# Optimization experiments

Measured on AMD Instinct MI355X. Metric: run time of the kernel, lower is better.

The kernel has to match this reference:

```python
import jax, jax.numpy as jnp
import numpy as np

D_MODEL = 1024
H = 16
D_K = D_MODEL // H


def setup_inputs() -> dict:
    key = jax.random.key(0)
    ks = jax.random.split(key, 9)
    s = 0.02
    x = jax.random.normal(ks[0], (2, 2048, D_MODEL), dtype=jnp.float32)
    Wq = jax.random.normal(ks[1], (D_MODEL, D_MODEL), dtype=jnp.float32) * s
    bq = jax.random.normal(ks[2], (D_MODEL,), dtype=jnp.float32) * s
    Wk = jax.random.normal(ks[3], (D_MODEL, D_MODEL), dtype=jnp.float32) * s
    bk = jax.random.normal(ks[4], (D_MODEL,), dtype=jnp.float32) * s
    Wv = jax.random.normal(ks[5], (D_MODEL, D_MODEL), dtype=jnp.float32) * s
    bv = jax.random.normal(ks[6], (D_MODEL,), dtype=jnp.float32) * s
    Wo = jax.random.normal(ks[7], (D_MODEL, D_MODEL), dtype=jnp.float32) * s
    bo = jax.random.normal(ks[8], (D_MODEL,), dtype=jnp.float32) * s
    return {"x": x, "Wq": Wq, "bq": bq, "Wk": Wk, "bk": bk,
            "Wv": Wv, "bv": bv, "Wo": Wo, "bo": bo}


def reference(x, Wq, bq, Wk, bk, Wv, bv, Wo, bo):
    b, s, _ = x.shape
    scale = 1.0 / jnp.sqrt(jnp.float32(D_K))
    # projections; [b, s, d] -> [b, h, s, d_k]
    def split_heads(t):
        return t.reshape(b, s, H, D_K).transpose(0, 2, 1, 3)
    q = split_heads(x @ Wq + bq)
    k = split_heads(x @ Wk + bk)
    v = split_heads(x @ Wv + bv)
    scores = jnp.einsum('bhqd,bhkd->bhqk', q, k) * scale  # [b,h,s,s]
    attn = jax.nn.softmax(scores, axis=-1)
    ctx = jnp.einsum('bhqk,bhkd->bhqd', attn, v)
    ctx = ctx.transpose(0, 2, 1, 3).reshape(b, s, D_MODEL)
    return ctx @ Wo + bo + x
```

## Files before the change

### kernel.cpp

```cpp
#include <hip/hip_runtime.h>
#include <hip/hip_bf16.h>
#include <stdint.h>

#define D_MODEL 1024
#define NH 16
#define DK 64
#define S_LEN 2048

typedef __attribute__((ext_vector_type(8))) __bf16 bf16x8;
typedef __attribute__((ext_vector_type(4))) float f32x4;

#define GLOBAL_AS __attribute__((address_space(1)))
#define LDS_AS    __attribute__((address_space(3)))

__device__ __forceinline__ void async16(const ushort* g, ushort* l) {
    __builtin_amdgcn_global_load_lds(
        (const GLOBAL_AS uint32_t*)(uintptr_t)(const void*)g,
        (LDS_AS uint32_t*)(uint32_t)(uintptr_t)(void*)l,
        16, 0, 0);
}

__device__ __forceinline__ ushort f2bf(float f) {
    union { float f; uint32_t u; } v; v.f = f;
    uint32_t lsb = (v.u >> 16) & 1u;
    return (ushort)((v.u + 0x7fffu + lsb) >> 16);
}

__device__ __forceinline__ uint32_t packbf(float a, float b) {
    union { float f; uint32_t u; } x, y; x.f = a; y.f = b;
    return ((x.u + 0x8000u) >> 16) | ((y.u + 0x8000u) & 0xffff0000u);
}

__device__ __forceinline__ bf16x8 ldfrag(const ushort* p) {
    union { uint4 u; bf16x8 b; } cv;
    cv.u = *(const uint4*)p;
    return cv.b;
}


__global__ void cvt_x_kernel(const float* __restrict__ x, ushort* __restrict__ xb) {
    int i = blockIdx.x * 256 + threadIdx.x;
    float4 v = ((const float4*)x)[i];
    ushort4 o;
    o.x = f2bf(v.x); o.y = f2bf(v.y); o.z = f2bf(v.z); o.w = f2bf(v.w);
    ((ushort4*)xb)[i] = o;
}

__global__ void transpose_cvt4_kernel(
    const float* __restrict__ W0, const float* __restrict__ W1,
    const float* __restrict__ W2, const float* __restrict__ W3,
    ushort* __restrict__ D0, ushort* __restrict__ D1,
    ushort* __restrict__ D2, ushort* __restrict__ D3) {
    const float* W; ushort* D;
    switch (blockIdx.z) {
        case 0: W = W0; D = D0; break;
        case 1: W = W1; D = D1; break;
        case 2: W = W2; D = D2; break;
        default: W = W3; D = D3; break;
    }
    __shared__ float tile[32][33];
    int bx = blockIdx.x * 32, by = blockIdx.y * 32;
    int tx = threadIdx.x, ty = threadIdx.y;
#pragma unroll
    for (int j = 0; j < 32; j += 8)
        tile[ty + j][tx] = W[(size_t)(by + ty + j) * D_MODEL + bx + tx];
    __syncthreads();
#pragma unroll
    for (int j = 0; j < 32; j += 8)
        D[(size_t)(bx + ty + j) * D_MODEL + by + tx] = f2bf(tile[tx][ty + j]);
}

__global__ void cvt_bias_kernel(const float* __restrict__ bq, const float* __restrict__ bk,
                                const float* __restrict__ bv, float* __restrict__ out) {
    int i = blockIdx.x * 256 + threadIdx.x;
    float v = (i < 1024) ? bq[i] : (i < 2048 ? bk[i - 1024] : bv[i - 2048]);
    out[i] = v;
}

template <int MODE>
__global__ __launch_bounds__(256) void gemm_kernel(
    const ushort* __restrict__ A, const ushort* __restrict__ Bt,
    const float* __restrict__ bias,
    ushort* __restrict__ outQ, ushort* __restrict__ outK, ushort* __restrict__ outVt,
    const float* __restrict__ xres, float* __restrict__ outF) {
    constexpr int BN = (MODE == 0) ? 128 : 64;
    constexpr int NI = (MODE == 0) ? 4 : 2;
    __shared__ __align__(16) ushort sA[2][128 * 32];
    __shared__ __align__(16) ushort sB[2][BN * 32];
    const int tid = threadIdx.x;
    const int wave = tid >> 6, lane = tid & 63;
    const int lr = lane & 15, lq = lane >> 4;
    const int srow = lane >> 2;
    const int sc = (lane & 3) ^ ((lane >> 4) & 3);

    const int bid = blockIdx.x;
    const int xcd = bid & 7, lb = bid >> 3;
    int bx, by;
    if (MODE == 0) { bx = xcd * 3 + (lb % 3); by = lb / 3; }
    else           { bx = xcd * 2 + (lb & 1); by = lb >> 1; }
    const int blockM = by * 128;
    const int blockN = bx * BN;
    const int waveM = (wave >> 1) * 64;
    const int waveN = (MODE == 0) ? (wave & 1) * 64 : (wave & 1) * 32;

    auto stage = [&](int k0, int b) {
#pragma unroll
        for (int t = 0; t < 2; t++) {
            int row = wave * 32 + t * 16 + srow;
            async16(&A[(size_t)(blockM + row) * D_MODEL + k0 + sc * 8],
                    &sA[b][(wave * 32 + t * 16) * 32]);
        }
        if (MODE == 0) {
#pragma unroll
            for (int t = 0; t < 2; t++) {
                int row = wave * 32 + t * 16 + srow;
                async16(&Bt[(size_t)(blockN + row) * D_MODEL + k0 + sc * 8],
                        &sB[b][(wave * 32 + t * 16) * 32]);
            }
        } else {
            int row = wave * 16 + srow;
            async16(&Bt[(size_t)(blockN + row) * D_MODEL + k0 + sc * 8],
                    &sB[b][wave * 16 * 32]);
        }
    };

    f32x4 acc[4][NI] = {};
    const int swz = (lq ^ ((lr >> 2) & 3)) * 8;

    stage(0, 0);
    __syncthreads();
#pragma unroll 2
    for (int k = 0; k < 32; k++) {
        const int cur = k & 1;
        if (k < 31) stage((k + 1) * 32, cur ^ 1);
        bf16x8 af[4], bfr[NI];
#pragma unroll
        for (int mi = 0; mi < 4; mi++)
            af[mi] = ldfrag(&sA[cur][(waveM + mi * 16 + lr) * 32 + swz]);
#pragma unroll
        for (int ni = 0; ni < NI; ni++)
            bfr[ni] = ldfrag(&sB[cur][(waveN + ni * 16 + lr) * 32 + swz]);
#pragma unroll
        for (int mi = 0; mi < 4; mi++)
#pragma unroll
            for (int ni = 0; ni < NI; ni++)
                acc[mi][ni] = __builtin_amdgcn_mfma_f32_16x16x32_bf16(
                    af[mi], bfr[ni], acc[mi][ni], 0, 0, 0);
        __syncthreads();
    }

#pragma unroll
    for (int mi = 0; mi < 4; mi++) {
#pragma unroll
        for (int ni = 0; ni < NI; ni++) {
#pragma unroll
            for (int r = 0; r < 4; r++) {
                int m = blockM + waveM + mi * 16 + lq * 4 + r;
                int n = blockN + waveN + ni * 16 + lr;
                float v = acc[mi][ni][r] + bias[n];
                if (MODE == 0) {
                    int which = n >> 10, c = n & 1023;
                    int h = c >> 6, d = c & 63;
                    int b = m >> 11, s = m & 2047;
                    size_t bh = (size_t)(b * NH + h);
                    if (which == 0)
                        outQ[(bh * S_LEN + s) * DK + d] = f2bf(v * 0.125f);
                    else if (which == 1)
                        outK[(bh * S_LEN + s) * DK + d] = f2bf(v);
                    else
                        outVt[(bh * DK + d) * S_LEN + s] = f2bf(v);
                } else {
                    size_t idx = (size_t)m * D_MODEL + n;
                    outF[idx] = v + xres[idx];
                }
            }
        }
    }
}

__global__ __launch_bounds__(256, 3) void attn_kernel(
    const ushort* __restrict__ Q, const ushort* __restrict__ Km,
    const ushort* __restrict__ Vt, ushort* __restrict__ ctx) {
    const int bid = blockIdx.x;
    const int xcd = bid & 7, lb = bid >> 3;
    const int bh = xcd * 4 + (lb & 3);
    const int qt = lb >> 2;
    const int q0 = qt * 128;
    __shared__ __align__(16) ushort sQ[128 * 64];
    __shared__ __align__(16) ushort sK[64 * 64];
    __shared__ __align__(16) ushort sV[64 * 64];
    __shared__ __align__(16) ushort sP[4 * 32 * 72];
    const int tid = threadIdx.x;
    const int wave = tid >> 6, lane = tid & 63;
    const int lr = lane & 15, lq = lane >> 4;
    const int srow = lane >> 3, sp = lane & 7;
    const ushort* Qh = Q + (size_t)bh * S_LEN * DK;
    const ushort* Kh = Km + (size_t)bh * S_LEN * DK;
    const ushort* Vh = Vt + (size_t)bh * DK * S_LEN;
    ushort* sPw = &sP[wave * 32 * 72];

#pragma unroll
    for (int t = 0; t < 4; t++) {
        int row = wave * 32 + t * 8 + srow;
        int c = sp ^ (row & 7);
        async16(&Qh[(size_t)(q0 + row) * DK + c * 8], &sQ[(wave * 32 + t * 8) * 64]);
    }
    __syncthreads();

    bf16x8 qf[2][2];
#pragma unroll
    for (int mi = 0; mi < 2; mi++)
#pragma unroll
        for (int kk = 0; kk < 2; kk++)
            qf[mi][kk] = ldfrag(&sQ[(wave * 32 + mi * 16 + lr) * 64 +
                                    (((kk * 4 + lq) ^ (lr & 7)) * 8)]);

    f32x4 cacc[2][4] = {};
    float lsum[2] = {0.f, 0.f};

    for (int k0 = 0; k0 < S_LEN; k0 += 64) {
        __syncthreads();
#pragma unroll
        for (int t = 0; t < 2; t++) {
            int row = wave * 16 + t * 8 + srow;
            int c = sp ^ (row & 7);
            async16(&Kh[(size_t)(k0 + row) * DK + c * 8], &sK[(wave * 16 + t * 8) * 64]);
            async16(&Vh[(size_t)row * S_LEN + k0 + c * 8], &sV[(wave * 16 + t * 8) * 64]);
        }
        __syncthreads();

        f32x4 sacc[2][4] = {};
#pragma unroll
        for (int kk = 0; kk < 2; kk++) {
            bf16x8 kf[4];
            int swz = ((kk * 4 + lq) ^ (lr & 7)) * 8;
#pragma unroll
            for (int nj = 0; nj < 4; nj++)
                kf[nj] = ldfrag(&sK[(nj * 16 + lr) * 64 + swz]);
#pragma unroll
            for (int mi = 0; mi < 2; mi++)
#pragma unroll
                for (int nj = 0; nj < 4; nj++)
                    sacc[mi][nj] = __builtin_amdgcn_mfma_f32_16x16x32_bf16(
                        kf[nj], qf[mi][kk], sacc[mi][nj], 0, 0, 0);
        }

#pragma unroll
        for (int mi = 0; mi < 2; mi++) {
#pragma unroll
            for (int nj = 0; nj < 4; nj++) {
                float p0 = __expf(sacc[mi][nj][0]);
                float p1 = __expf(sacc[mi][nj][1]);
                float p2 = __expf(sacc[mi][nj][2]);
                float p3 = __expf(sacc[mi][nj][3]);
                lsum[mi] += (p0 + p1) + (p2 + p3);
                uint2 w;
                w.x = packbf(p0, p1);
                w.y = packbf(p2, p3);
                *(uint2*)&sPw[(mi * 16 + lr) * 72 + nj * 16 + lq * 4] = w;
            }
        }

#pragma unroll
        for (int ks = 0; ks < 2; ks++) {
            bf16x8 pf[2], vf[4];
#pragma unroll
            for (int mi = 0; mi < 2; mi++)
                pf[mi] = ldfrag(&sPw[(mi * 16 + lr) * 72 + ks * 32 + lq * 8]);
            int swz = ((ks * 4 + lq) ^ (lr & 7)) * 8;
#pragma unroll
            for (int nd = 0; nd < 4; nd++)
                vf[nd] = ldfrag(&sV[(nd * 16 + lr) * 64 + swz]);
#pragma unroll
            for (int mi = 0; mi < 2; mi++)
#pragma unroll
                for (int nd = 0; nd < 4; nd++)
                    cacc[mi][nd] = __builtin_amdgcn_mfma_f32_16x16x32_bf16(
                        pf[mi], vf[nd], cacc[mi][nd], 0, 0, 0);
        }
    }

    float inv[2];
#pragma unroll
    for (int mi = 0; mi < 2; mi++) {
        float l = lsum[mi];
        l += __shfl_xor(l, 16);
        l += __shfl_xor(l, 32);
        inv[mi] = 1.f / l;
    }
    float invr[2][4];
#pragma unroll
    for (int mi = 0; mi < 2; mi++)
#pragma unroll
        for (int r = 0; r < 4; r++)
            invr[mi][r] = __shfl(inv[mi], lq * 4 + r);

    const int b = bh >> 4, h = bh & 15;
#pragma unroll
    for (int mi = 0; mi < 2; mi++)
#pragma unroll
        for (int nd = 0; nd < 4; nd++)
#pragma unroll
            for (int r = 0; r < 4; r++) {
                int qrow = q0 + wave * 32 + mi * 16 + lq * 4 + r;
                int d = nd * 16 + lr;
                float v = cacc[mi][nd][r] * invr[mi][r];
                ctx[(size_t)(b * S_LEN + qrow) * D_MODEL + h * DK + d] = f2bf(v);
            }
}


extern "C" void kernel_launch(void* const* d_in, const int* in_sizes, int n_in,
                              void* d_out, int out_size, void* d_ws, size_t ws_size,
                              hipStream_t stream) {
    const float* x  = (const float*)d_in[0];
    const float* Wq = (const float*)d_in[1];
    const float* bq = (const float*)d_in[2];
    const float* Wk = (const float*)d_in[3];
    const float* bk = (const float*)d_in[4];
    const float* Wv = (const float*)d_in[5];
    const float* bv = (const float*)d_in[6];
    const float* Wo = (const float*)d_in[7];
    const float* bo = (const float*)d_in[8];

    char* ws = (char*)d_ws;
    ushort* xb    = (ushort*)(ws);
    ushort* wqkv  = (ushort*)(ws + (8ull  << 20));
    ushort* wo_t  = (ushort*)(ws + (14ull << 20));
    ushort* qbuf  = (ushort*)(ws + (16ull << 20));
    ushort* kbuf  = (ushort*)(ws + (24ull << 20));
    ushort* vtb   = (ushort*)(ws + (32ull << 20));
    ushort* ctx   = (ushort*)(ws + (40ull << 20));
    float*  biasq = (float*)(ws + (48ull << 20));

    cvt_x_kernel<<<4096, 256, 0, stream>>>(x, xb);
    transpose_cvt4_kernel<<<dim3(32, 32, 4), dim3(32, 8), 0, stream>>>(
        Wq, Wk, Wv, Wo, wqkv, wqkv + 1024 * 1024, wqkv + 2 * 1024 * 1024, wo_t);
    cvt_bias_kernel<<<12, 256, 0, stream>>>(bq, bk, bv, biasq);

    gemm_kernel<0><<<768, 256, 0, stream>>>(
        xb, wqkv, biasq, qbuf, kbuf, vtb, nullptr, nullptr);
    attn_kernel<<<512, 256, 0, stream>>>(qbuf, kbuf, vtb, ctx);
    gemm_kernel<1><<<512, 256, 0, stream>>>(
        ctx, wo_t, bo, nullptr, nullptr, nullptr, x, (float*)d_out);
}
```

Measured before the change: 216.5 us.

## Triple-buffer GEMMs, halve attention q-tile, use exp2 and MFMA row sums

The GEMM kernel moves from two to three LDS stages. It prefetches two k-steps ahead and replaces __syncthreads with a vmcnt-bounded barrier, and the output-projection block mapping is remapped across XCDs. The attention kernel shrinks the query tile to 64 rows with 16 per wave and reuses the Q LDS slot for P. It folds log2(e) into the Q scale so it can use a raw v_exp_f32, and computes softmax row sums with an extra MFMA against a ones vector in place of scalar adds and shuffles. The aims are more overlap of loads with MFMA, more blocks for occupancy, and less VALU work. In exchange K/V traffic per query doubles, and the vmcnt counts must match the number of loads issued.

```diff
diff --git a/kernel.cpp b/kernel.cpp
--- a/kernel.cpp
+++ b/kernel.cpp
@@ -18,6 +18,17 @@
         (const GLOBAL_AS uint32_t*)(uintptr_t)(const void*)g,
         (LDS_AS uint32_t*)(uint32_t)(uintptr_t)(void*)l,
         16, 0, 0);
+}
+
+template <int N>
+__device__ __forceinline__ void pipe_barrier() {
+    asm volatile("s_waitcnt vmcnt(%0)\n\ts_barrier" :: "n"(N) : "memory");
+}
+
+__device__ __forceinline__ float fast_exp2(float x) {
+    float r;
+    asm("v_exp_f32 %0, %1" : "=v"(r) : "v"(x));
+    return r;
 }
 
 __device__ __forceinline__ ushort f2bf(float f) {
@@ -85,8 +96,9 @@
     const float* __restrict__ xres, float* __restrict__ outF) {
     constexpr int BN = (MODE == 0) ? 128 : 64;
     constexpr int NI = (MODE == 0) ? 4 : 2;
-    __shared__ __align__(16) ushort sA[2][128 * 32];
-    __shared__ __align__(16) ushort sB[2][BN * 32];
+    constexpr int NS = (MODE == 0) ? 4 : 3;
+    __shared__ __align__(16) ushort sA[3][128 * 32];
+    __shared__ __align__(16) ushort sB[3][BN * 32];
     const int tid = threadIdx.x;
     const int wave = tid >> 6, lane = tid & 63;
     const int lr = lane & 15, lq = lane >> 4;
@@ -97,56 +109,63 @@
     const int xcd = bid & 7, lb = bid >> 3;
     int bx, by;
     if (MODE == 0) { bx = xcd * 3 + (lb % 3); by = lb / 3; }
-    else           { bx = xcd * 2 + (lb & 1); by = lb >> 1; }
+    else           { by = xcd * 4 + (lb & 3); bx = lb >> 2; }
     const int blockM = by * 128;
     const int blockN = bx * BN;
     const int waveM = (wave >> 1) * 64;
     const int waveN = (MODE == 0) ? (wave & 1) * 64 : (wave & 1) * 32;
 
-    auto stage = [&](int k0, int b) {
+    auto stage = [&](int k0, ushort* a, ushort* b) {
 #pragma unroll
         for (int t = 0; t < 2; t++) {
             int row = wave * 32 + t * 16 + srow;
             async16(&A[(size_t)(blockM + row) * D_MODEL + k0 + sc * 8],
-                    &sA[b][(wave * 32 + t * 16) * 32]);
+                    &a[(wave * 32 + t * 16) * 32]);
         }
         if (MODE == 0) {
 #pragma unroll
             for (int t = 0; t < 2; t++) {
                 int row = wave * 32 + t * 16 + srow;
                 async16(&Bt[(size_t)(blockN + row) * D_MODEL + k0 + sc * 8],
-                        &sB[b][(wave * 32 + t * 16) * 32]);
+                        &b[(wave * 32 + t * 16) * 32]);
             }
         } else {
             int row = wave * 16 + srow;
             async16(&Bt[(size_t)(blockN + row) * D_MODEL + k0 + sc * 8],
-                    &sB[b][wave * 16 * 32]);
+                    &b[wave * 16 * 32]);
         }
     };
 
     f32x4 acc[4][NI] = {};
     const int swz = (lq ^ ((lr >> 2) & 3)) * 8;
 
-    stage(0, 0);
+    stage(0, sA[0], sB[0]);
+    stage(32, sA[1], sB[1]);
     __syncthreads();
-#pragma unroll 2
+
+    int cur = 0;
+#pragma unroll 4
     for (int k = 0; k < 32; k++) {
-        const int cur = k & 1;
-        if (k < 31) stage((k + 1) * 32, cur ^ 1);
+        int nx = cur + 2; if (nx >= 3) nx -= 3;
+        if (k + 2 < 32) stage((k + 2) * 32, sA[nx], sB[nx]);
+        const ushort* a = sA[cur];
+        const ushort* b = sB[cur];
         bf16x8 af[4], bfr[NI];
 #pragma unroll
         for (int mi = 0; mi < 4; mi++)
-            af[mi] = ldfrag(&sA[cur][(waveM + mi * 16 + lr) * 32 + swz]);
+            af[mi] = ldfrag(&a[(waveM + mi * 16 + lr) * 32 + swz]);
 #pragma unroll
         for (int ni = 0; ni < NI; ni++)
-            bfr[ni] = ldfrag(&sB[cur][(waveN + ni * 16 + lr) * 32 + swz]);
+            bfr[ni] = ldfrag(&b[(waveN + ni * 16 + lr) * 32 + swz]);
 #pragma unroll
         for (int mi = 0; mi < 4; mi++)
 #pragma unroll
             for (int ni = 0; ni < NI; ni++)
                 acc[mi][ni] = __builtin_amdgcn_mfma_f32_16x16x32_bf16(
                     af[mi], bfr[ni], acc[mi][ni], 0, 0, 0);
-        __syncthreads();
+        if (k < 30) pipe_barrier<NS>();
+        else if (k == 30) pipe_barrier<0>();
+        cur = (cur == 2) ? 0 : cur + 1;
     }
 
 #pragma unroll
@@ -161,10 +180,10 @@
                 if (MODE == 0) {
                     int which = n >> 10, c = n & 1023;
                     int h = c >> 6, d = c & 63;
-                    int b = m >> 11, s = m & 2047;
-                    size_t bh = (size_t)(b * NH + h);
+                    int b2 = m >> 11, s = m & 2047;
+                    size_t bh = (size_t)(b2 * NH + h);
                     if (which == 0)
-                        outQ[(bh * S_LEN + s) * DK + d] = f2bf(v * 0.125f);
+                        outQ[(bh * S_LEN + s) * DK + d] = f2bf(v * 0.1803368801f);
                     else if (which == 1)
                         outK[(bh * S_LEN + s) * DK + d] = f2bf(v);
                     else
@@ -178,18 +197,17 @@
     }
 }
 
-__global__ __launch_bounds__(256, 3) void attn_kernel(
+__global__ __launch_bounds__(256, 4) void attn_kernel(
     const ushort* __restrict__ Q, const ushort* __restrict__ Km,
     const ushort* __restrict__ Vt, ushort* __restrict__ ctx) {
     const int bid = blockIdx.x;
     const int xcd = bid & 7, lb = bid >> 3;
     const int bh = xcd * 4 + (lb & 3);
     const int qt = lb >> 2;
-    const int q0 = qt * 128;
-    __shared__ __align__(16) ushort sQ[128 * 64];
+    const int q0 = qt * 64;
+    __shared__ __align__(16) ushort sQP[4][16 * 64];
     __shared__ __align__(16) ushort sK[64 * 64];
     __shared__ __align__(16) ushort sV[64 * 64];
-    __shared__ __align__(16) ushort sP[4 * 32 * 72];
     const int tid = threadIdx.x;
     const int wave = tid >> 6, lane = tid & 63;
     const int lr = lane & 15, lq = lane >> 4;
@@ -197,26 +215,28 @@
     const ushort* Qh = Q + (size_t)bh * S_LEN * DK;
     const ushort* Kh = Km + (size_t)bh * S_LEN * DK;
     const ushort* Vh = Vt + (size_t)bh * DK * S_LEN;
-    ushort* sPw = &sP[wave * 32 * 72];
-
-#pragma unroll
-    for (int t = 0; t < 4; t++) {
-        int row = wave * 32 + t * 8 + srow;
+    ushort* sPw = sQP[wave];
+
+#pragma unroll
+    for (int t = 0; t < 2; t++) {
+        int row = t * 8 + srow;
         int c = sp ^ (row & 7);
-        async16(&Qh[(size_t)(q0 + row) * DK + c * 8], &sQ[(wave * 32 + t * 8) * 64]);
+        async16(&Qh[(size_t)(q0 + wave * 16 + row) * DK + c * 8],
+                &sPw[t * 8 * 64]);
     }
     __syncthreads();
 
-    bf16x8 qf[2][2];
-#pragma unroll
-    for (int mi = 0; mi < 2; mi++)
-#pragma unroll
-        for (int kk = 0; kk < 2; kk++)
-            qf[mi][kk] = ldfrag(&sQ[(wave * 32 + mi * 16 + lr) * 64 +
-                                    (((kk * 4 + lq) ^ (lr & 7)) * 8)]);
-
-    f32x4 cacc[2][4] = {};
-    float lsum[2] = {0.f, 0.f};
+    bf16x8 qf[2];
+#pragma unroll
+    for (int kk = 0; kk < 2; kk++)
+        qf[kk] = ldfrag(&sPw[lr * 64 + (((kk * 4 + lq) ^ (lr & 7)) * 8)]);
+
+    union { uint4 u; bf16x8 b; } one_u;
+    one_u.u = make_uint4(0x3F803F80u, 0x3F803F80u, 0x3F803F80u, 0x3F803F80u);
+    const bf16x8 ones = one_u.b;
+
+    f32x4 cacc[4] = {};
+    f32x4 ssum = {};
 
     for (int k0 = 0; k0 < S_LEN; k0 += 64) {
         __syncthreads();
@@ -229,84 +249,58 @@
         }
         __syncthreads();
 
-        f32x4 sacc[2][4] = {};
+        f32x4 sacc[4] = {};
 #pragma unroll
         for (int kk = 0; kk < 2; kk++) {
-            bf16x8 kf[4];
             int swz = ((kk * 4 + lq) ^ (lr & 7)) * 8;
 #pragma unroll
-            for (int nj = 0; nj < 4; nj++)
-                kf[nj] = ldfrag(&sK[(nj * 16 + lr) * 64 + swz]);
-#pragma unroll
-            for (int mi = 0; mi < 2; mi++)
-#pragma unroll
-                for (int nj = 0; nj < 4; nj++)
-                    sacc[mi][nj] = __builtin_amdgcn_mfma_f32_16x16x32_bf16(
-                        kf[nj], qf[mi][kk], sacc[mi][nj], 0, 0, 0);
-        }
-
-#pragma unroll
-        for (int mi = 0; mi < 2; mi++) {
-#pragma unroll
             for (int nj = 0; nj < 4; nj++) {
-                float p0 = __expf(sacc[mi][nj][0]);
-                float p1 = __expf(sacc[mi][nj][1]);
-                float p2 = __expf(sacc[mi][nj][2]);
-                float p3 = __expf(sacc[mi][nj][3]);
-                lsum[mi] += (p0 + p1) + (p2 + p3);
-                uint2 w;
-                w.x = packbf(p0, p1);
-                w.y = packbf(p2, p3);
-                *(uint2*)&sPw[(mi * 16 + lr) * 72 + nj * 16 + lq * 4] = w;
+                bf16x8 kf = ldfrag(&sK[(nj * 16 + lr) * 64 + swz]);
+                sacc[nj] = __builtin_amdgcn_mfma_f32_16x16x32_bf16(
+                    kf, qf[kk], sacc[nj], 0, 0, 0);
             }
         }
 
 #pragma unroll
+        for (int nj = 0; nj < 4; nj++) {
+            float p0 = fast_exp2(sacc[nj][0]);
+            float p1 = fast_exp2(sacc[nj][1]);
+            float p2 = fast_exp2(sacc[nj][2]);
+            float p3 = fast_exp2(sacc[nj][3]);
+            uint2 w;
+            w.x = packbf(p0, p1);
+            w.y = packbf(p2, p3);
+            int physc = (nj * 2 + (lq >> 1)) ^ (lr & 7);
+            *(uint2*)&sPw[lr * 64 + physc * 8 + (lq & 1) * 4] = w;
+        }
+
+#pragma unroll
         for (int ks = 0; ks < 2; ks++) {
-            bf16x8 pf[2], vf[4];
-#pragma unroll
-            for (int mi = 0; mi < 2; mi++)
-                pf[mi] = ldfrag(&sPw[(mi * 16 + lr) * 72 + ks * 32 + lq * 8]);
+            bf16x8 pf = ldfrag(&sPw[lr * 64 + (((ks * 4 + lq) ^ (lr & 7)) * 8)]);
             int swz = ((ks * 4 + lq) ^ (lr & 7)) * 8;
 #pragma unroll
-            for (int nd = 0; nd < 4; nd++)
-                vf[nd] = ldfrag(&sV[(nd * 16 + lr) * 64 + swz]);
-#pragma unroll
-            for (int mi = 0; mi < 2; mi++)
-#pragma unroll
-                for (int nd = 0; nd < 4; nd++)
-                    cacc[mi][nd] = __builtin_amdgcn_mfma_f32_16x16x32_bf16(
-                        pf[mi], vf[nd], cacc[mi][nd], 0, 0, 0);
-        }
-    }
-
-    float inv[2];
-#pragma unroll
-    for (int mi = 0; mi < 2; mi++) {
-        float l = lsum[mi];
-        l += __shfl_xor(l, 16);
-        l += __shfl_xor(l, 32);
-        inv[mi] = 1.f / l;
-    }
-    float invr[2][4];
-#pragma unroll
-    for (int mi = 0; mi < 2; mi++)
-#pragma unroll
-        for (int r = 0; r < 4; r++)
-            invr[mi][r] = __shfl(inv[mi], lq * 4 + r);
+            for (int nd = 0; nd < 4; nd++) {
+                bf16x8 vf = ldfrag(&sV[(nd * 16 + lr) * 64 + swz]);
+                cacc[nd] = __builtin_amdgcn_mfma_f32_16x16x32_bf16(
+                    pf, vf, cacc[nd], 0, 0, 0);
+            }
+            ssum = __builtin_amdgcn_mfma_f32_16x16x32_bf16(pf, ones, ssum, 0, 0, 0);
+        }
+    }
 
     const int b = bh >> 4, h = bh & 15;
-#pragma unroll
-    for (int mi = 0; mi < 2; mi++)
-#pragma unroll
-        for (int nd = 0; nd < 4; nd++)
-#pragma unroll
-            for (int r = 0; r < 4; r++) {
-                int qrow = q0 + wave * 32 + mi * 16 + lq * 4 + r;
-                int d = nd * 16 + lr;
-                float v = cacc[mi][nd][r] * invr[mi][r];
-                ctx[(size_t)(b * S_LEN + qrow) * D_MODEL + h * DK + d] = f2bf(v);
-            }
+    float inv[4];
+#pragma unroll
+    for (int r = 0; r < 4; r++) inv[r] = __builtin_amdgcn_rcpf(ssum[r]);
+#pragma unroll
+    for (int nd = 0; nd < 4; nd++)
+#pragma unroll
+        for (int r = 0; r < 4; r++) {
+            int qrow = q0 + wave * 16 + lq * 4 + r;
+            int d = nd * 16 + lr;
+            float v = cacc[nd][r] * inv[r];
+            ctx[(size_t)(b * S_LEN + qrow) * D_MODEL + h * DK + d] = f2bf(v);
+        }
 }
 
 
@@ -340,7 +334,7 @@
 
     gemm_kernel<0><<<768, 256, 0, stream>>>(
         xb, wqkv, biasq, qbuf, kbuf, vtb, nullptr, nullptr);
-    attn_kernel<<<512, 256, 0, stream>>>(qbuf, kbuf, vtb, ctx);
+    attn_kernel<<<1024, 256, 0, stream>>>(qbuf, kbuf, vtb, ctx);
     gemm_kernel<1><<<512, 256, 0, stream>>>(
         ctx, wo_t, bo, nullptr, nullptr, nullptr, x, (float*)d_out);
 }
```

After: 217.6 us. No clear change (+0.5%).
